# Kernel optimization log

Hardware: AMD Instinct MI355X
Metric: run time of the kernel (lower is better)

Reference implementation:

```python
import jax, jax.numpy as jnp
import numpy as np

EMBED = 1024
HEADS = 16
HEAD_DIM = EMBED // HEADS
MLP_HIDDEN = 4096


def _layernorm(x, g, b, eps=1e-5):
    mu = jnp.mean(x, axis=-1, keepdims=True)
    var = jnp.mean(jnp.square(x - mu), axis=-1, keepdims=True)
    return (x - mu) * jax.lax.rsqrt(var + eps) * g + b


def setup_inputs() -> dict:
    key = jax.random.key(0)
    ks = jax.random.split(key, 8)
    s = 0.02
    return {
        "x": jax.random.normal(ks[0], (8, 1024, EMBED), dtype=jnp.float32),
        "qkv_w": jax.random.normal(ks[1], (EMBED, 3 * EMBED), dtype=jnp.float32) * s,
        "qkv_b": jnp.zeros((3 * EMBED,), jnp.float32),
        "proj_w": jax.random.normal(ks[2], (EMBED, EMBED), dtype=jnp.float32) * s,
        "proj_b": jnp.zeros((EMBED,), jnp.float32),
        "fc1_w": jax.random.normal(ks[3], (EMBED, MLP_HIDDEN), dtype=jnp.float32) * s,
        "fc1_b": jnp.zeros((MLP_HIDDEN,), jnp.float32),
        "fc2_w": jax.random.normal(ks[4], (MLP_HIDDEN, EMBED), dtype=jnp.float32) * s,
        "fc2_b": jnp.zeros((EMBED,), jnp.float32),
        "ln1_g": jnp.ones((EMBED,), jnp.float32),
        "ln1_b": jnp.zeros((EMBED,), jnp.float32),
        "ln2_g": jnp.ones((EMBED,), jnp.float32),
        "ln2_b": jnp.zeros((EMBED,), jnp.float32),
    }


def reference(x, qkv_w, qkv_b, proj_w, proj_b, fc1_w, fc1_b, fc2_w, fc2_b,
              ln1_g, ln1_b, ln2_g, ln2_b):
    B, N, C = x.shape
    scale = HEAD_DIM ** -0.5

    # --- MHSA on pre-norm input ---
    h = _layernorm(x, ln1_g, ln1_b)
    qkv = h @ qkv_w + qkv_b                      # [B,N,3C]
    qkv = qkv.reshape(B, N, 3, HEADS, HEAD_DIM)
    q, k, v = (qkv[:, :, i].transpose(0, 2, 1, 3) for i in range(3))  # [B,H,N,d]
    attn = jnp.einsum('bhqd,bhkd->bhqk', q, k) * scale
    attn = jax.nn.softmax(attn, axis=-1)
    o = jnp.einsum('bhqk,bhkd->bhqd', attn, v)   # [B,H,N,d]
    o = o.transpose(0, 2, 1, 3).reshape(B, N, C)
    x = x + (o @ proj_w + proj_b)

    # --- MLP ---
    h2 = _layernorm(x, ln2_g, ln2_b)
    h2 = jax.nn.gelu(h2 @ fc1_w + fc1_b, approximate=False)
    x = x + (h2 @ fc2_w + fc2_b)
    return x
```

## Files before the change

### kernel.cpp

```cpp
#include <hip/hip_runtime.h>
#include <hip/hip_bf16.h>

typedef __bf16 bf16x8 __attribute__((ext_vector_type(8)));
typedef float  f32x4  __attribute__((ext_vector_type(4)));
typedef unsigned short u16;

static __device__ __forceinline__ u16 f2bf(float f) {
  union { float f; unsigned u; } v; v.f = f;
  unsigned r = v.u + 0x7fffu + ((v.u >> 16) & 1u);
  return (u16)(r >> 16);
}

static __device__ __forceinline__ void gld16(const void* g, void* l) {
  __builtin_amdgcn_global_load_lds(
      (const __attribute__((address_space(1))) unsigned int*)g,
      (__attribute__((address_space(3))) unsigned int*)l, 16, 0, 0);
}

#define SBAR() do { __builtin_amdgcn_sched_barrier(0); \
                    __builtin_amdgcn_s_barrier(); \
                    __builtin_amdgcn_sched_barrier(0); } while (0)

__global__ __launch_bounds__(256) void transpose_cast_k(
    const float* __restrict__ W, u16* __restrict__ Wt, int K, int N) {
  __shared__ float tile[32][33];
  const int t = threadIdx.x;
  const int n0 = blockIdx.x * 32, k0 = blockIdx.y * 32;
  const int r = t >> 3, c4 = (t & 7) * 4;
  const float4 v = *(const float4*)(W + (size_t)(k0 + r) * N + n0 + c4);
  tile[r][c4 + 0] = v.x; tile[r][c4 + 1] = v.y;
  tile[r][c4 + 2] = v.z; tile[r][c4 + 3] = v.w;
  __syncthreads();
  const int n = t >> 3, k4 = (t & 7) * 4;
  uint2 pk;
  pk.x = f2bf(tile[k4 + 0][n]) | ((unsigned)f2bf(tile[k4 + 1][n]) << 16);
  pk.y = f2bf(tile[k4 + 2][n]) | ((unsigned)f2bf(tile[k4 + 3][n]) << 16);
  *(uint2*)(Wt + (size_t)(n0 + n) * K + k0 + k4) = pk;
}

__global__ __launch_bounds__(256) void ln_cast_k(
    const float* __restrict__ x, const float* __restrict__ g,
    const float* __restrict__ b, u16* __restrict__ out) {
  __shared__ float red[2][4];
  const int t = threadIdx.x;
  const size_t row = blockIdx.x;
  const float4 v = *(const float4*)(x + row * 1024 + t * 4);
  float s = v.x + v.y + v.z + v.w;
  float ss = v.x * v.x + v.y * v.y + v.z * v.z + v.w * v.w;
  #pragma unroll
  for (int m = 1; m <= 32; m <<= 1) { s += __shfl_xor(s, m); ss += __shfl_xor(ss, m); }
  if ((t & 63) == 0) { red[0][t >> 6] = s; red[1][t >> 6] = ss; }
  __syncthreads();
  s  = red[0][0] + red[0][1] + red[0][2] + red[0][3];
  ss = red[1][0] + red[1][1] + red[1][2] + red[1][3];
  const float mu = s * (1.f / 1024.f);
  const float var = ss * (1.f / 1024.f) - mu * mu;
  const float rs = rsqrtf(var + 1e-5f);
  const float4 gv = *(const float4*)(g + t * 4);
  const float4 bv = *(const float4*)(b + t * 4);
  uint2 pk;
  pk.x = f2bf((v.x - mu) * rs * gv.x + bv.x) |
         ((unsigned)f2bf((v.y - mu) * rs * gv.y + bv.y) << 16);
  pk.y = f2bf((v.z - mu) * rs * gv.z + bv.z) |
         ((unsigned)f2bf((v.w - mu) * rs * gv.w + bv.w) << 16);
  *(uint2*)(out + row * 1024 + t * 4) = pk;
}

template <int EPI, int WN>
__global__ __launch_bounds__(512, 2) void gemm8_k(
    const u16* __restrict__ A, const u16* __restrict__ Bt,
    const float* __restrict__ bias, u16* __restrict__ Cb, float* __restrict__ Cf,
    const float* __restrict__ R, u16* __restrict__ vT, int M, int N, int K) {
  constexpr int MR = 2 * WN;
  constexpr int BN = 64 * WN;
  constexpr int SHSZ = 32768 + WN * 8192;
  __shared__ u16 SH[SHSZ];
  const int t = threadIdx.x;
  const int nt = N / BN;
  const int q = gridDim.x >> 3;
  const int swz = (blockIdx.x & 7) * q + (blockIdx.x >> 3);
  const int tn = swz % nt, tm = swz / nt;
  const int lo = t & 15, hi = (t >> 4) & 3, wid = t >> 6;
  const int wm = wid / WN, wn = wid & (WN - 1);
  const int NT = K >> 6;

  const int srow = t >> 3;
  const int sc = (t & 7) ^ (srow & 7);
  const u16* gA = A  + (size_t)(tm * 256) * K;
  const u16* gB = Bt + (size_t)(tn * BN) * K;
  auto stA = [&](int dd, int c, int T) {
    gld16(gA + (size_t)(c * 64 + srow) * K + (size_t)T * 64 + sc * 8,
          &SH[dd * 16384 + c * 4096 + t * 8]);
  };
  auto stB = [&](int dd, int c, int T) {
    gld16(gB + (size_t)(c * 64 + srow) * K + (size_t)T * 64 + sc * 8,
          &SH[32768 + dd * (WN * 4096) + c * 4096 + t * 8]);
  };

  const int xr = lo & 7;
  const int rowA = wm * (MR * 16) + lo;
  const int rowB = wn * 64 + lo;
#define RD_A(d, m, kk) (*(const bf16x8*)&SH[(d)*16384 + (rowA + (m)*16)*64 + ((((kk)<<2)+hi)^xr)*8])
#define RD_B(d, n, kk) (*(const bf16x8*)&SH[32768 + (d)*(WN*4096) + (rowB + (n)*16)*64 + ((((kk)<<2)+hi)^xr)*8])
#define MF(a, b, c) __builtin_amdgcn_mfma_f32_16x16x32_bf16(a, b, c, 0, 0, 0)

  f32x4 acc[MR][4];
  #pragma unroll
  for (int i = 0; i < MR; ++i)
    #pragma unroll
    for (int j = 0; j < 4; ++j) acc[i][j] = (f32x4){0.f, 0.f, 0.f, 0.f};

#define PH16(d, M0, M1, STAGES, WAITS) do { \
    bf16x8 a0 = RD_A(d, M0, 0), a1 = RD_A(d, M0, 1); \
    bf16x8 a2 = RD_A(d, M1, 0), a3 = RD_A(d, M1, 1); \
    STAGES; SBAR(); __builtin_amdgcn_s_setprio(1); \
    acc[M0][0]=MF(a0,b00,acc[M0][0]); acc[M0][1]=MF(a0,b10,acc[M0][1]); \
    acc[M0][2]=MF(a0,b20,acc[M0][2]); acc[M0][3]=MF(a0,b30,acc[M0][3]); \
    acc[M1][0]=MF(a2,b00,acc[M1][0]); acc[M1][1]=MF(a2,b10,acc[M1][1]); \
    acc[M1][2]=MF(a2,b20,acc[M1][2]); acc[M1][3]=MF(a2,b30,acc[M1][3]); \
    acc[M0][0]=MF(a1,b01,acc[M0][0]); acc[M0][1]=MF(a1,b11,acc[M0][1]); \
    acc[M0][2]=MF(a1,b21,acc[M0][2]); acc[M0][3]=MF(a1,b31,acc[M0][3]); \
    acc[M1][0]=MF(a3,b01,acc[M1][0]); acc[M1][1]=MF(a3,b11,acc[M1][1]); \
    acc[M1][2]=MF(a3,b21,acc[M1][2]); acc[M1][3]=MF(a3,b31,acc[M1][3]); \
    __builtin_amdgcn_s_setprio(0); WAITS; SBAR(); } while (0)

#define PH8(d, M0, STAGES, WAITS) do { \
    bf16x8 a0 = RD_A(d, M0, 0), a1 = RD_A(d, M0, 1); \
    STAGES; SBAR(); __builtin_amdgcn_s_setprio(1); \
    acc[M0][0]=MF(a0,b00,acc[M0][0]); acc[M0][1]=MF(a0,b10,acc[M0][1]); \
    acc[M0][2]=MF(a0,b20,acc[M0][2]); acc[M0][3]=MF(a0,b30,acc[M0][3]); \
    acc[M0][0]=MF(a1,b01,acc[M0][0]); acc[M0][1]=MF(a1,b11,acc[M0][1]); \
    acc[M0][2]=MF(a1,b21,acc[M0][2]); acc[M0][3]=MF(a1,b31,acc[M0][3]); \
    __builtin_amdgcn_s_setprio(0); WAITS; SBAR(); } while (0)

  if constexpr (WN == 4) {
    stA(0, 0, 0); stA(0, 1, 0); stA(0, 2, 0); stA(0, 3, 0);
    stB(0, 0, 0); stB(0, 1, 0); stB(0, 2, 0); stB(0, 3, 0);
    stB(1, 0, 1); stB(1, 1, 1); stB(1, 2, 1); stB(1, 3, 1);
    stA(1, 0, 1); stA(1, 2, 1);
    asm volatile("s_waitcnt vmcnt(6)" ::: "memory");
    SBAR();
    for (int T = 0; T < NT; ++T) {
      const int d = T & 1, dn = d ^ 1;
      bf16x8 b00 = RD_B(d,0,0), b01 = RD_B(d,0,1), b10 = RD_B(d,1,0), b11 = RD_B(d,1,1);
      bf16x8 b20 = RD_B(d,2,0), b21 = RD_B(d,2,1), b30 = RD_B(d,3,0), b31 = RD_B(d,3,1);
      PH16(d, 0, 1, { if (T + 1 < NT) { stA(dn, 1, T + 1); stA(dn, 3, T + 1); } }, );
      PH16(d, 2, 3, { if (T + 2 < NT) { stB(d, 0, T + 2); stB(d, 1, T + 2); } }, );
      PH16(d, 4, 5, { if (T + 2 < NT) { stB(d, 2, T + 2); stB(d, 3, T + 2); } }, );
      PH16(d, 6, 7, { if (T + 2 < NT) { stA(d, 0, T + 2); stA(d, 2, T + 2); } },
           { if (T < NT - 2)       { asm volatile("s_waitcnt vmcnt(6)" ::: "memory"); }
             else if (T == NT - 2) { asm volatile("s_waitcnt vmcnt(0)" ::: "memory"); } });
    }
  } else {
    stA(0, 0, 0); stA(0, 1, 0); stA(0, 2, 0); stA(0, 3, 0);
    stB(0, 0, 0); stB(0, 1, 0);
    stB(1, 0, 1); stB(1, 1, 1);
    asm volatile("s_waitcnt vmcnt(2)" ::: "memory");
    SBAR();
    for (int T = 0; T < NT; ++T) {
      const int d = T & 1, dn = d ^ 1;
      bf16x8 b00 = RD_B(d,0,0), b01 = RD_B(d,0,1), b10 = RD_B(d,1,0), b11 = RD_B(d,1,1);
      bf16x8 b20 = RD_B(d,2,0), b21 = RD_B(d,2,1), b30 = RD_B(d,3,0), b31 = RD_B(d,3,1);
      PH8(d, 0, { if (T + 1 < NT) { stA(dn, 0, T + 1); stA(dn, 1, T + 1);
                                    stA(dn, 2, T + 1); stA(dn, 3, T + 1); } }, );
      PH8(d, 1, { if (T + 2 < NT) { stB(d, 0, T + 2); stB(d, 1, T + 2); } }, );
      PH8(d, 2, , );
      PH8(d, 3, ,
          { if (T < NT - 2)       { asm volatile("s_waitcnt vmcnt(2)" ::: "memory"); }
            else if (T == NT - 2) { asm volatile("s_waitcnt vmcnt(0)" ::: "memory"); } });
    }
  }

  if constexpr (EPI == 2) {
    #pragma unroll
    for (int ni = 0; ni < 4; ++ni) {
      const int col = tn * BN + wn * 64 + ni * 16 + lo;
      const float bv = bias[col];
      #pragma unroll
      for (int mi = 0; mi < MR; ++mi) {
        const int row0 = tm * 256 + wm * (MR * 16) + mi * 16 + hi * 4;
        #pragma unroll
        for (int r = 0; r < 4; ++r) {
          const size_t idx = (size_t)(row0 + r) * N + col;
          Cf[idx] = acc[mi][ni][r] + bv + R[idx];
        }
      }
    }
  } else {
    #pragma unroll
    for (int ni = 0; ni < 4; ++ni) {
      const int colL = wn * 64 + ni * 16 + lo;
      const float bv = bias[tn * BN + colL];
      #pragma unroll
      for (int mi = 0; mi < MR; ++mi) {
        const int rowL = wm * (MR * 16) + mi * 16 + hi * 4;
        #pragma unroll
        for (int r = 0; r < 4; ++r) {
          float val = acc[mi][ni][r] + bv;
          if (EPI == 1) {
            const float u = 0.79788456f * val * (1.f + 0.044715f * val * val);
            const float e = __expf(fminf(2.f * u, 80.f));
            val = val * (e / (e + 1.f));
          }
          SH[(rowL + r) * BN + colL] = f2bf(val);
        }
      }
    }
    __syncthreads();
    constexpr int ROWSH = (BN == 256) ? 9 : 8;
    const int base = t * 16;
    #pragma unroll
    for (int p = 0; p < BN / 16; ++p) {
      const int o = base + p * 8192;
      const int row = o >> ROWSH;
      const int cb = (o & (2 * BN - 1)) >> 1;
      const uint4 v4 = *(const uint4*)&SH[o >> 1];
      *(uint4*)(Cb + (size_t)(tm * 256 + row) * N + tn * BN + cb) = v4;
    }
    if constexpr (EPI == 3) {
      if (tn >= 8) {
        const int c = t & 255;
        const int rg = t >> 8;
        const int gcol = tn * 256 + c;
        const int hh = (gcol - 2048) >> 6, dd = gcol & 63;
        const int bb = tm >> 2, nb = (tm & 3) * 256;
        u16* dst = vT + ((size_t)((bb * 16 + hh) * 64 + dd) << 10) + nb + rg * 128;
        #pragma unroll
        for (int i = 0; i < 16; ++i) {
          const int r0 = rg * 128 + i * 8;
          u16 tv[8];
          #pragma unroll
          for (int j = 0; j < 8; ++j) tv[j] = SH[(r0 + j) * 256 + c];
          uint4 pk;
          pk.x = tv[0] | ((unsigned)tv[1] << 16);
          pk.y = tv[2] | ((unsigned)tv[3] << 16);
          pk.z = tv[4] | ((unsigned)tv[5] << 16);
          pk.w = tv[6] | ((unsigned)tv[7] << 16);
          *(uint4*)(dst + i * 8) = pk;
        }
      }
    }
  }
#undef RD_A
#undef RD_B
#undef MF
#undef PH16
#undef PH8
}

__global__ __launch_bounds__(256, 2) void attn_k(
    const u16* __restrict__ qkv, const u16* __restrict__ vT, u16* __restrict__ o) {
  __shared__ u16 lK[64 * 64];
  __shared__ u16 lV[64 * 64];
  __shared__ u16 lP[64 * 72];
  const int t = threadIdx.x;
  const int lo = t & 15, hi = (t >> 4) & 3, w = t >> 6;
  const int swz = (blockIdx.x & 7) * 256 + (blockIdx.x >> 3);
  const int qt = swz & 15, bh = swz >> 4;
  const int b = bh >> 4, h = bh & 15;
  const int q0 = qt * 64;
  const u16* Qb = qkv + (size_t)b * 1024 * 3072 + h * 64;
  const u16* Kb = Qb + 1024;
  const u16* Vt = vT + (size_t)bh * 64 * 1024;

  bf16x8 qf[2];
  {
    const size_t q = q0 + w * 16 + lo;
    qf[0] = *(const bf16x8*)(Qb + q * 3072 + hi * 8);
    qf[1] = *(const bf16x8*)(Qb + q * 3072 + 32 + hi * 8);
  }
  f32x4 oacc[4];
  #pragma unroll
  for (int i = 0; i < 4; ++i) oacc[i] = (f32x4){0.f, 0.f, 0.f, 0.f};
  float m = -1e30f, lsum = 0.f;
  const int srow = t >> 3;
  const int sc = (t & 7) ^ (srow & 7);
  const int xr = lo & 7;
  const float SC = 0.125f * 1.44269504f;

  for (int kv0 = 0; kv0 < 1024; kv0 += 64) {
    __syncthreads();
    #pragma unroll
    for (int j = 0; j < 2; ++j) {
      const int r64 = j * 32 + srow;
      gld16(Kb + (size_t)(kv0 + r64) * 3072 + sc * 8, &lK[(j * 256 + t) * 8]);
      gld16(Vt + (size_t)r64 * 1024 + kv0 + sc * 8, &lV[(j * 256 + t) * 8]);
    }
    __syncthreads();

    f32x4 s[4];
    #pragma unroll
    for (int i = 0; i < 4; ++i) s[i] = (f32x4){0.f, 0.f, 0.f, 0.f};
    #pragma unroll
    for (int kk = 0; kk < 2; ++kk) {
      #pragma unroll
      for (int mi = 0; mi < 4; ++mi) {
        const bf16x8 kf = *(const bf16x8*)&lK[(mi * 16 + lo) * 64 + (((kk << 2) + hi) ^ xr) * 8];
        s[mi] = __builtin_amdgcn_mfma_f32_16x16x32_bf16(kf, qf[kk], s[mi], 0, 0, 0);
      }
    }
    float sv[16];
    float tmax = -1e30f;
    #pragma unroll
    for (int mi = 0; mi < 4; ++mi)
      #pragma unroll
      for (int r = 0; r < 4; ++r) {
        const float xx = s[mi][r] * SC;
        sv[mi * 4 + r] = xx;
        tmax = fmaxf(tmax, xx);
      }
    tmax = fmaxf(tmax, __shfl_xor(tmax, 16));
    tmax = fmaxf(tmax, __shfl_xor(tmax, 32));
    if (__any(tmax > m + 11.5f)) {
      const float mnew = fmaxf(m, tmax);
      const float alpha = exp2f(m - mnew);
      m = mnew;
      lsum *= alpha;
      float ar[4];
      #pragma unroll
      for (int r = 0; r < 4; ++r) ar[r] = __shfl(alpha, hi * 4 + r);
      #pragma unroll
      for (int ni = 0; ni < 4; ++ni)
        #pragma unroll
        for (int r = 0; r < 4; ++r) oacc[ni][r] *= ar[r];
    }
    float p[16], ts = 0.f;
    #pragma unroll
    for (int i = 0; i < 16; ++i) { p[i] = exp2f(sv[i] - m); ts += p[i]; }
    ts += __shfl_xor(ts, 16);
    ts += __shfl_xor(ts, 32);
    lsum += ts;
    #pragma unroll
    for (int mi = 0; mi < 4; ++mi) {
      uint2 pk;
      pk.x = f2bf(p[mi * 4 + 0]) | ((unsigned)f2bf(p[mi * 4 + 1]) << 16);
      pk.y = f2bf(p[mi * 4 + 2]) | ((unsigned)f2bf(p[mi * 4 + 3]) << 16);
      *(uint2*)&lP[(w * 16 + lo) * 72 + mi * 16 + hi * 4] = pk;
    }
    asm volatile("s_waitcnt lgkmcnt(0)" ::: "memory");
    #pragma unroll
    for (int kk = 0; kk < 2; ++kk) {
      const bf16x8 pf = *(const bf16x8*)&lP[(w * 16 + lo) * 72 + kk * 32 + hi * 8];
      #pragma unroll
      for (int ni = 0; ni < 4; ++ni) {
        const bf16x8 vf = *(const bf16x8*)&lV[(ni * 16 + lo) * 64 + (((kk << 2) + hi) ^ xr) * 8];
        oacc[ni] = __builtin_amdgcn_mfma_f32_16x16x32_bf16(pf, vf, oacc[ni], 0, 0, 0);
      }
    }
  }
  float lr[4];
  #pragma unroll
  for (int r = 0; r < 4; ++r) lr[r] = 1.f / __shfl(lsum, hi * 4 + r);
  #pragma unroll
  for (int ni = 0; ni < 4; ++ni) {
    const int d = ni * 16 + lo;
    #pragma unroll
    for (int r = 0; r < 4; ++r) {
      const int n = q0 + w * 16 + hi * 4 + r;
      o[((size_t)(b * 1024 + n) * 16 + h) * 64 + d] = f2bf(oacc[ni][r] * lr[r]);
    }
  }
}

extern "C" void kernel_launch(void* const* d_in, const int* in_sizes, int n_in,
                              void* d_out, int out_size, void* d_ws, size_t ws_size,
                              hipStream_t stream) {
  const float* x      = (const float*)d_in[0];
  const float* qkv_w  = (const float*)d_in[1];
  const float* qkv_b  = (const float*)d_in[2];
  const float* proj_w = (const float*)d_in[3];
  const float* proj_b = (const float*)d_in[4];
  const float* fc1_w  = (const float*)d_in[5];
  const float* fc1_b  = (const float*)d_in[6];
  const float* fc2_w  = (const float*)d_in[7];
  const float* fc2_b  = (const float*)d_in[8];
  const float* ln1_g  = (const float*)d_in[9];
  const float* ln1_b  = (const float*)d_in[10];
  const float* ln2_g  = (const float*)d_in[11];
  const float* ln2_b  = (const float*)d_in[12];
  float* out = (float*)d_out;
  char* ws = (char*)d_ws;
  u16* wqkvT = (u16*)(ws);
  u16* wprojT = (u16*)(ws + 6291456);
  u16* wfc1T = (u16*)(ws + 8388608);
  u16* wfc2T = (u16*)(ws + 16777216);
  u16* hbuf  = (u16*)(ws + 25165824);
  u16* qkvo  = (u16*)(ws + 41943040);
  u16* vT    = (u16*)(ws + 92274688);
  u16* fc1o  = qkvo;

  transpose_cast_k<<<dim3(96, 32),  256, 0, stream>>>(qkv_w,  wqkvT, 1024, 3072);
  transpose_cast_k<<<dim3(32, 32),  256, 0, stream>>>(proj_w, wprojT, 1024, 1024);
  transpose_cast_k<<<dim3(128, 32), 256, 0, stream>>>(fc1_w,  wfc1T, 1024, 4096);
  transpose_cast_k<<<dim3(32, 128), 256, 0, stream>>>(fc2_w,  wfc2T, 4096, 1024);
  ln_cast_k<<<8192, 256, 0, stream>>>(x, ln1_g, ln1_b, hbuf);
  gemm8_k<3, 4><<<384, 512, 0, stream>>>(hbuf, wqkvT, qkv_b, qkvo, nullptr, nullptr, vT, 8192, 3072, 1024);
  attn_k<<<2048, 256, 0, stream>>>(qkvo, vT, hbuf);
  gemm8_k<2, 2><<<256, 512, 0, stream>>>(hbuf, wprojT, proj_b, nullptr, out, x, nullptr, 8192, 1024, 1024);
  ln_cast_k<<<8192, 256, 0, stream>>>(out, ln2_g, ln2_b, hbuf);
  gemm8_k<1, 4><<<512, 512, 0, stream>>>(hbuf, wfc1T, fc1_b, fc1o, nullptr, nullptr, nullptr, 8192, 4096, 1024);
  gemm8_k<2, 2><<<256, 512, 0, stream>>>(fc1o, wfc2T, fc2_b, nullptr, out, out, nullptr, 8192, 1024, 4096);
}
```

Before: 384.0 us.

## Merge prep kernels and replace hand-scheduled GEMM pipeline with simpler double buffer

```diff
diff --git a/kernel.cpp b/kernel.cpp
--- a/kernel.cpp
+++ b/kernel.cpp
@@ -21,21 +21,57 @@
                     __builtin_amdgcn_s_barrier(); \
                     __builtin_amdgcn_sched_barrier(0); } while (0)
 
-__global__ __launch_bounds__(256) void transpose_cast_k(
-    const float* __restrict__ W, u16* __restrict__ Wt, int K, int N) {
-  __shared__ float tile[32][33];
+__global__ __launch_bounds__(256) void prep_k(
+    const float* __restrict__ qkv_w, const float* __restrict__ proj_w,
+    const float* __restrict__ fc1_w, const float* __restrict__ fc2_w,
+    u16* __restrict__ wqkvT, u16* __restrict__ wprojT,
+    u16* __restrict__ wfc1T, u16* __restrict__ wfc2T,
+    const float* __restrict__ x, const float* __restrict__ g,
+    const float* __restrict__ b, u16* __restrict__ hbuf) {
+  const int bid = blockIdx.x;
   const int t = threadIdx.x;
-  const int n0 = blockIdx.x * 32, k0 = blockIdx.y * 32;
-  const int r = t >> 3, c4 = (t & 7) * 4;
-  const float4 v = *(const float4*)(W + (size_t)(k0 + r) * N + n0 + c4);
-  tile[r][c4 + 0] = v.x; tile[r][c4 + 1] = v.y;
-  tile[r][c4 + 2] = v.z; tile[r][c4 + 3] = v.w;
-  __syncthreads();
-  const int n = t >> 3, k4 = (t & 7) * 4;
-  uint2 pk;
-  pk.x = f2bf(tile[k4 + 0][n]) | ((unsigned)f2bf(tile[k4 + 1][n]) << 16);
-  pk.y = f2bf(tile[k4 + 2][n]) | ((unsigned)f2bf(tile[k4 + 3][n]) << 16);
-  *(uint2*)(Wt + (size_t)(n0 + n) * K + k0 + k4) = pk;
+  if (bid < 12288) {
+    __shared__ float tile[32][33];
+    const float* W; u16* Wt; int K, N, nx, i;
+    if (bid < 3072)      { W = qkv_w;  Wt = wqkvT;  K = 1024; N = 3072; nx = 96;  i = bid; }
+    else if (bid < 4096) { W = proj_w; Wt = wprojT; K = 1024; N = 1024; nx = 32;  i = bid - 3072; }
+    else if (bid < 8192) { W = fc1_w;  Wt = wfc1T;  K = 1024; N = 4096; nx = 128; i = bid - 4096; }
+    else                 { W = fc2_w;  Wt = wfc2T;  K = 4096; N = 1024; nx = 32;  i = bid - 8192; }
+    const int n0 = (i % nx) * 32, k0 = (i / nx) * 32;
+    const int r = t >> 3, c4 = (t & 7) * 4;
+    const float4 v = *(const float4*)(W + (size_t)(k0 + r) * N + n0 + c4);
+    tile[r][c4 + 0] = v.x; tile[r][c4 + 1] = v.y;
+    tile[r][c4 + 2] = v.z; tile[r][c4 + 3] = v.w;
+    __syncthreads();
+    const int n = t >> 3, k4 = (t & 7) * 4;
+    uint2 pk;
+    pk.x = f2bf(tile[k4 + 0][n]) | ((unsigned)f2bf(tile[k4 + 1][n]) << 16);
+    pk.y = f2bf(tile[k4 + 2][n]) | ((unsigned)f2bf(tile[k4 + 3][n]) << 16);
+    *(uint2*)(Wt + (size_t)(n0 + n) * K + k0 + k4) = pk;
+  } else {
+    __shared__ float red[2][4];
+    const size_t row = bid - 12288;
+    const float4 v = *(const float4*)(x + row * 1024 + t * 4);
+    float s = v.x + v.y + v.z + v.w;
+    float ss = v.x * v.x + v.y * v.y + v.z * v.z + v.w * v.w;
+    #pragma unroll
+    for (int m = 1; m <= 32; m <<= 1) { s += __shfl_xor(s, m); ss += __shfl_xor(ss, m); }
+    if ((t & 63) == 0) { red[0][t >> 6] = s; red[1][t >> 6] = ss; }
+    __syncthreads();
+    s  = red[0][0] + red[0][1] + red[0][2] + red[0][3];
+    ss = red[1][0] + red[1][1] + red[1][2] + red[1][3];
+    const float mu = s * (1.f / 1024.f);
+    const float var = ss * (1.f / 1024.f) - mu * mu;
+    const float rs = rsqrtf(var + 1e-5f);
+    const float4 gv = *(const float4*)(g + t * 4);
+    const float4 bv = *(const float4*)(b + t * 4);
+    uint2 pk;
+    pk.x = f2bf((v.x - mu) * rs * gv.x + bv.x) |
+           ((unsigned)f2bf((v.y - mu) * rs * gv.y + bv.y) << 16);
+    pk.y = f2bf((v.z - mu) * rs * gv.z + bv.z) |
+           ((unsigned)f2bf((v.w - mu) * rs * gv.w + bv.w) << 16);
+    *(uint2*)(hbuf + row * 1024 + t * 4) = pk;
+  }
 }
 
 __global__ __launch_bounds__(256) void ln_cast_k(
@@ -67,14 +103,14 @@
 }
 
 template <int EPI, int WN>
-__global__ __launch_bounds__(512, 2) void gemm8_k(
+__global__ __launch_bounds__(512, 1) void gemm_k(
     const u16* __restrict__ A, const u16* __restrict__ Bt,
     const float* __restrict__ bias, u16* __restrict__ Cb, float* __restrict__ Cf,
     const float* __restrict__ R, u16* __restrict__ vT, int M, int N, int K) {
   constexpr int MR = 2 * WN;
+  constexpr int MPP = MR / 4;
   constexpr int BN = 64 * WN;
-  constexpr int SHSZ = 32768 + WN * 8192;
-  __shared__ u16 SH[SHSZ];
+  __shared__ u16 SH[32768 + WN * 8192];
   const int t = threadIdx.x;
   const int nt = N / BN;
   const int q = gridDim.x >> 3;
@@ -88,13 +124,15 @@
   const int sc = (t & 7) ^ (srow & 7);
   const u16* gA = A  + (size_t)(tm * 256) * K;
   const u16* gB = Bt + (size_t)(tn * BN) * K;
-  auto stA = [&](int dd, int c, int T) {
-    gld16(gA + (size_t)(c * 64 + srow) * K + (size_t)T * 64 + sc * 8,
-          &SH[dd * 16384 + c * 4096 + t * 8]);
-  };
-  auto stB = [&](int dd, int c, int T) {
-    gld16(gB + (size_t)(c * 64 + srow) * K + (size_t)T * 64 + sc * 8,
-          &SH[32768 + dd * (WN * 4096) + c * 4096 + t * 8]);
+  auto STAGE = [&](int dd, int T) {
+    #pragma unroll
+    for (int c = 0; c < 4; ++c)
+      gld16(gA + (size_t)(c * 64 + srow) * K + (size_t)T * 64 + sc * 8,
+            &SH[dd * 16384 + c * 4096 + t * 8]);
+    #pragma unroll
+    for (int c = 0; c < WN; ++c)
+      gld16(gB + (size_t)(c * 64 + srow) * K + (size_t)T * 64 + sc * 8,
+            &SH[32768 + dd * (WN * 4096) + c * 4096 + t * 8]);
   };
 
   const int xr = lo & 7;
@@ -110,65 +148,55 @@
     #pragma unroll
     for (int j = 0; j < 4; ++j) acc[i][j] = (f32x4){0.f, 0.f, 0.f, 0.f};
 
-#define PH16(d, M0, M1, STAGES, WAITS) do { \
-    bf16x8 a0 = RD_A(d, M0, 0), a1 = RD_A(d, M0, 1); \
-    bf16x8 a2 = RD_A(d, M1, 0), a3 = RD_A(d, M1, 1); \
-    STAGES; SBAR(); __builtin_amdgcn_s_setprio(1); \
-    acc[M0][0]=MF(a0,b00,acc[M0][0]); acc[M0][1]=MF(a0,b10,acc[M0][1]); \
-    acc[M0][2]=MF(a0,b20,acc[M0][2]); acc[M0][3]=MF(a0,b30,acc[M0][3]); \
-    acc[M1][0]=MF(a2,b00,acc[M1][0]); acc[M1][1]=MF(a2,b10,acc[M1][1]); \
-    acc[M1][2]=MF(a2,b20,acc[M1][2]); acc[M1][3]=MF(a2,b30,acc[M1][3]); \
-    acc[M0][0]=MF(a1,b01,acc[M0][0]); acc[M0][1]=MF(a1,b11,acc[M0][1]); \
-    acc[M0][2]=MF(a1,b21,acc[M0][2]); acc[M0][3]=MF(a1,b31,acc[M0][3]); \
-    acc[M1][0]=MF(a3,b01,acc[M1][0]); acc[M1][1]=MF(a3,b11,acc[M1][1]); \
-    acc[M1][2]=MF(a3,b21,acc[M1][2]); acc[M1][3]=MF(a3,b31,acc[M1][3]); \
-    __builtin_amdgcn_s_setprio(0); WAITS; SBAR(); } while (0)
-
-#define PH8(d, M0, STAGES, WAITS) do { \
-    bf16x8 a0 = RD_A(d, M0, 0), a1 = RD_A(d, M0, 1); \
-    STAGES; SBAR(); __builtin_amdgcn_s_setprio(1); \
-    acc[M0][0]=MF(a0,b00,acc[M0][0]); acc[M0][1]=MF(a0,b10,acc[M0][1]); \
-    acc[M0][2]=MF(a0,b20,acc[M0][2]); acc[M0][3]=MF(a0,b30,acc[M0][3]); \
-    acc[M0][0]=MF(a1,b01,acc[M0][0]); acc[M0][1]=MF(a1,b11,acc[M0][1]); \
-    acc[M0][2]=MF(a1,b21,acc[M0][2]); acc[M0][3]=MF(a1,b31,acc[M0][3]); \
-    __builtin_amdgcn_s_setprio(0); WAITS; SBAR(); } while (0)
-
-  if constexpr (WN == 4) {
-    stA(0, 0, 0); stA(0, 1, 0); stA(0, 2, 0); stA(0, 3, 0);
-    stB(0, 0, 0); stB(0, 1, 0); stB(0, 2, 0); stB(0, 3, 0);
-    stB(1, 0, 1); stB(1, 1, 1); stB(1, 2, 1); stB(1, 3, 1);
-    stA(1, 0, 1); stA(1, 2, 1);
-    asm volatile("s_waitcnt vmcnt(6)" ::: "memory");
+  bf16x8 bF[8];
+  bf16x8 aP[MPP * 2], aQ[MPP * 2];
+
+  auto LDA = [&](bf16x8* arr, int d, int p) {
+    #pragma unroll
+    for (int ml = 0; ml < MPP; ++ml) {
+      arr[ml * 2 + 0] = RD_A(d, p * MPP + ml, 0);
+      arr[ml * 2 + 1] = RD_A(d, p * MPP + ml, 1);
+    }
+  };
+  auto LDB = [&](int d) {
+    #pragma unroll
+    for (int n = 0; n < 4; ++n) {
+      bF[n * 2 + 0] = RD_B(d, n, 0);
+      bF[n * 2 + 1] = RD_B(d, n, 1);
+    }
+  };
+  auto DOMF = [&](bf16x8* arr, int p) {
+    __builtin_amdgcn_s_setprio(1);
+    #pragma unroll
+    for (int kk = 0; kk < 2; ++kk)
+      #pragma unroll
+      for (int ml = 0; ml < MPP; ++ml) {
+        const int m = p * MPP + ml;
+        #pragma unroll
+        for (int n = 0; n < 4; ++n)
+          acc[m][n] = MF(arr[ml * 2 + kk], bF[n * 2 + kk], acc[m][n]);
+      }
+    __builtin_amdgcn_s_setprio(0);
+  };
+
+  STAGE(0, 0);
+  asm volatile("s_waitcnt vmcnt(0)" ::: "memory");
+  SBAR();
+
+  for (int T = 0; T < NT; ++T) {
+    const int d = T & 1, dn = d ^ 1;
+    LDA(aP, d, 0);
+    if (T + 1 < NT) STAGE(dn, T + 1);
+    LDB(d);
+    LDA(aQ, d, 1);
+    DOMF(aP, 0);
+    LDA(aP, d, 2);
+    DOMF(aQ, 1);
+    LDA(aQ, d, 3);
+    DOMF(aP, 2);
+    DOMF(aQ, 3);
+    if (T + 1 < NT) { asm volatile("s_waitcnt vmcnt(0)" ::: "memory"); }
     SBAR();
-    for (int T = 0; T < NT; ++T) {
-      const int d = T & 1, dn = d ^ 1;
-      bf16x8 b00 = RD_B(d,0,0), b01 = RD_B(d,0,1), b10 = RD_B(d,1,0), b11 = RD_B(d,1,1);
-      bf16x8 b20 = RD_B(d,2,0), b21 = RD_B(d,2,1), b30 = RD_B(d,3,0), b31 = RD_B(d,3,1);
-      PH16(d, 0, 1, { if (T + 1 < NT) { stA(dn, 1, T + 1); stA(dn, 3, T + 1); } }, );
-      PH16(d, 2, 3, { if (T + 2 < NT) { stB(d, 0, T + 2); stB(d, 1, T + 2); } }, );
-      PH16(d, 4, 5, { if (T + 2 < NT) { stB(d, 2, T + 2); stB(d, 3, T + 2); } }, );
-      PH16(d, 6, 7, { if (T + 2 < NT) { stA(d, 0, T + 2); stA(d, 2, T + 2); } },
-           { if (T < NT - 2)       { asm volatile("s_waitcnt vmcnt(6)" ::: "memory"); }
-             else if (T == NT - 2) { asm volatile("s_waitcnt vmcnt(0)" ::: "memory"); } });
-    }
-  } else {
-    stA(0, 0, 0); stA(0, 1, 0); stA(0, 2, 0); stA(0, 3, 0);
-    stB(0, 0, 0); stB(0, 1, 0);
-    stB(1, 0, 1); stB(1, 1, 1);
-    asm volatile("s_waitcnt vmcnt(2)" ::: "memory");
-    SBAR();
-    for (int T = 0; T < NT; ++T) {
-      const int d = T & 1, dn = d ^ 1;
-      bf16x8 b00 = RD_B(d,0,0), b01 = RD_B(d,0,1), b10 = RD_B(d,1,0), b11 = RD_B(d,1,1);
-      bf16x8 b20 = RD_B(d,2,0), b21 = RD_B(d,2,1), b30 = RD_B(d,3,0), b31 = RD_B(d,3,1);
-      PH8(d, 0, { if (T + 1 < NT) { stA(dn, 0, T + 1); stA(dn, 1, T + 1);
-                                    stA(dn, 2, T + 1); stA(dn, 3, T + 1); } }, );
-      PH8(d, 1, { if (T + 2 < NT) { stB(d, 0, T + 2); stB(d, 1, T + 2); } }, );
-      PH8(d, 2, , );
-      PH8(d, 3, ,
-          { if (T < NT - 2)       { asm volatile("s_waitcnt vmcnt(2)" ::: "memory"); }
-            else if (T == NT - 2) { asm volatile("s_waitcnt vmcnt(0)" ::: "memory"); } });
-    }
   }
 
   if constexpr (EPI == 2) {
@@ -244,8 +272,6 @@
 #undef RD_A
 #undef RD_B
 #undef MF
-#undef PH16
-#undef PH8
 }
 
 __global__ __launch_bounds__(256, 2) void attn_k(
@@ -389,15 +415,13 @@
   u16* vT    = (u16*)(ws + 92274688);
   u16* fc1o  = qkvo;
 
-  transpose_cast_k<<<dim3(96, 32),  256, 0, stream>>>(qkv_w,  wqkvT, 1024, 3072);
-  transpose_cast_k<<<dim3(32, 32),  256, 0, stream>>>(proj_w, wprojT, 1024, 1024);
-  transpose_cast_k<<<dim3(128, 32), 256, 0, stream>>>(fc1_w,  wfc1T, 1024, 4096);
-  transpose_cast_k<<<dim3(32, 128), 256, 0, stream>>>(fc2_w,  wfc2T, 4096, 1024);
-  ln_cast_k<<<8192, 256, 0, stream>>>(x, ln1_g, ln1_b, hbuf);
-  gemm8_k<3, 4><<<384, 512, 0, stream>>>(hbuf, wqkvT, qkv_b, qkvo, nullptr, nullptr, vT, 8192, 3072, 1024);
+  prep_k<<<20480, 256, 0, stream>>>(qkv_w, proj_w, fc1_w, fc2_w,
+                                    wqkvT, wprojT, wfc1T, wfc2T,
+                                    x, ln1_g, ln1_b, hbuf);
+  gemm_k<3, 4><<<384, 512, 0, stream>>>(hbuf, wqkvT, qkv_b, qkvo, nullptr, nullptr, vT, 8192, 3072, 1024);
   attn_k<<<2048, 256, 0, stream>>>(qkvo, vT, hbuf);
-  gemm8_k<2, 2><<<256, 512, 0, stream>>>(hbuf, wprojT, proj_b, nullptr, out, x, nullptr, 8192, 1024, 1024);
+  gemm_k<2, 2><<<256, 512, 0, stream>>>(hbuf, wprojT, proj_b, nullptr, out, x, nullptr, 8192, 1024, 1024);
   ln_cast_k<<<8192, 256, 0, stream>>>(out, ln2_g, ln2_b, hbuf);
-  gemm8_k<1, 4><<<512, 512, 0, stream>>>(hbuf, wfc1T, fc1_b, fc1o, nullptr, nullptr, nullptr, 8192, 4096, 1024);
-  gemm8_k<2, 2><<<256, 512, 0, stream>>>(fc1o, wfc2T, fc2_b, nullptr, out, out, nullptr, 8192, 1024, 4096);
-}
+  gemm_k<1, 4><<<512, 512, 0, stream>>>(hbuf, wfc1T, fc1_b, fc1o, nullptr, nullptr, nullptr, 8192, 4096, 1024);
+  gemm_k<2, 2><<<256, 512, 0, stream>>>(fc1o, wfc2T, fc2_b, nullptr, out, out, nullptr, 8192, 1024, 4096);
+}
```

Measured after the change: 374.3 us. 2.5% less time.
